# Optimization experiments

Hardware: AMD Instinct MI355X
Metric: run time of the kernel (lower is better)

Reference implementation:

```python
import jax, jax.numpy as jnp
import numpy as np

TOP_K = 2  # matches init_kwargs top_k


def setup_inputs() -> dict:
    key = jax.random.key(0)
    ks = jax.random.split(key, 5)
    B, T, C, H, E = 4, 1024, 768, 3072, 8
    x = jax.random.normal(ks[0], (B, T, C), dtype=jnp.float32)
    Wg = jax.random.normal(ks[1], (C, E), dtype=jnp.float32) * 0.02
    W1 = jax.random.normal(ks[2], (E, C, H), dtype=jnp.float32) * (1.0 / np.sqrt(C))
    b1 = jnp.zeros((E, H), dtype=jnp.float32)
    W2 = jax.random.normal(ks[3], (E, H, C), dtype=jnp.float32) * (1.0 / np.sqrt(H))
    b2 = jnp.zeros((E, C), dtype=jnp.float32)
    return {"x": x, "Wg": Wg, "W1": W1, "b1": b1, "W2": W2, "b2": b2}


def reference(x, Wg, W1, b1, W2, b2):
    # TopKRouter: softmax over expert logits, keep top-k probs, zeros elsewhere.
    E = Wg.shape[-1]
    logits = jnp.einsum('btc,ce->bte', x, Wg)
    probs = jax.nn.softmax(logits, axis=-1)
    top_vals, top_idx = jax.lax.top_k(probs, TOP_K)          # (B,T,K)
    gates = (jax.nn.one_hot(top_idx, E, dtype=probs.dtype) * top_vals[..., None]).sum(-2)  # (B,T,E)

    # Per-expert FFN (Linear -> ReLU -> Linear; dropout is identity in eval),
    # combined with sparse gate weights (only top-k entries are nonzero).
    h = jax.nn.relu(jnp.einsum('btc,ech->bteh', x, W1) + b1)  # (B,T,E,H)
    y = jnp.einsum('bteh,ehc->btec', h, W2) + b2              # (B,T,E,C)
    out = jnp.einsum('bte,btec->btc', gates, y)               # (B,T,C)
    return out
```

## Files before the change

### kernel.cpp

```cpp
#include <hip/hip_runtime.h>
#include <hip/hip_bf16.h>
#include <cmath>

#define NT    4096
#define CDIM  768
#define HDIM  3072
#define NEXP  8
#define CAP   1280

typedef __bf16 bf16_t;
typedef __bf16 bf16x8 __attribute__((ext_vector_type(8)));
typedef float  f32x4  __attribute__((ext_vector_type(4)));

__device__ __forceinline__ void glds16(const void* g, void* l) {
    __builtin_amdgcn_global_load_lds(
        (const __attribute__((address_space(1))) void*)g,
        (__attribute__((address_space(3))) void*)l, 16, 0, 0);
}

template<int R, int CC>
__global__ __launch_bounds__(256)
void transpose_convert_kernel(const float* __restrict__ in, bf16_t* __restrict__ out) {
    __shared__ float tile[64][68];
    int e = blockIdx.z;
    int c0 = blockIdx.x * 64, r0 = blockIdx.y * 64;
    const float* src = in + (size_t)e * R * CC;
    bf16_t* dst = out + (size_t)e * R * CC;
    int t = threadIdx.x;
    int c4 = (t & 15) * 4, rr = t >> 4;
    #pragma unroll
    for (int i = 0; i < 4; i++) {
        int r = rr + i * 16;
        float4 v = *reinterpret_cast<const float4*>(&src[(size_t)(r0 + r) * CC + c0 + c4]);
        tile[r][c4 + 0] = v.x; tile[r][c4 + 1] = v.y;
        tile[r][c4 + 2] = v.z; tile[r][c4 + 3] = v.w;
    }
    __syncthreads();
    #pragma unroll
    for (int i = 0; i < 4; i++) {
        int cc = rr + i * 16;
        int r4 = (t & 15) * 4;
        union { bf16_t h[4]; uint2 u; } un;
        un.h[0] = (bf16_t)tile[r4 + 0][cc]; un.h[1] = (bf16_t)tile[r4 + 1][cc];
        un.h[2] = (bf16_t)tile[r4 + 2][cc]; un.h[3] = (bf16_t)tile[r4 + 3][cc];
        *reinterpret_cast<uint2*>(&dst[(size_t)(c0 + cc) * R + r0 + r4]) = un.u;
    }
}

__global__ __launch_bounds__(512)
void router_kernel(const float* __restrict__ x, const float* __restrict__ wg,
                   bf16_t* __restrict__ xb,
                   int* __restrict__ counts, int* __restrict__ tmap,
                   float* __restrict__ gmap, int* __restrict__ smap) {
    __shared__ int lcnt[NEXP];
    __shared__ int gbase[NEXP];
    int tid = threadIdx.x, lane = tid & 63, wid = tid >> 6;
    if (tid < NEXP) lcnt[tid] = 0;
    __syncthreads();

    int ti0[4], ti1[4], tr0[4], tr1[4];
    float tg0[4], tg1[4];

    #pragma unroll
    for (int k = 0; k < 4; k++) {
        int t = blockIdx.x * 32 + wid * 4 + k;
        const float* xr = x + (size_t)t * CDIM;
        float acc[NEXP];
        #pragma unroll
        for (int e = 0; e < NEXP; e++) acc[e] = 0.f;
        #pragma unroll
        for (int i = 0; i < CDIM / 256; i++) {
            int c = (i * 64 + lane) * 4;
            float4 v = *reinterpret_cast<const float4*>(xr + c);
            union { bf16_t h[4]; uint2 u; } un;
            un.h[0] = (bf16_t)v.x; un.h[1] = (bf16_t)v.y;
            un.h[2] = (bf16_t)v.z; un.h[3] = (bf16_t)v.w;
            *reinterpret_cast<uint2*>(xb + (size_t)t * CDIM + c) = un.u;
            float vv[4] = {v.x, v.y, v.z, v.w};
            #pragma unroll
            for (int j = 0; j < 4; j++)
                #pragma unroll
                for (int e = 0; e < NEXP; e++)
                    acc[e] += vv[j] * wg[(c + j) * NEXP + e];
        }
        #pragma unroll
        for (int e = 0; e < NEXP; e++) {
            #pragma unroll
            for (int off = 32; off > 0; off >>= 1)
                acc[e] += __shfl_xor(acc[e], off, 64);
        }
        if (lane == 0) {
            float mx = acc[0];
            #pragma unroll
            for (int e = 1; e < NEXP; e++) mx = fmaxf(mx, acc[e]);
            float p[NEXP], s = 0.f;
            #pragma unroll
            for (int e = 0; e < NEXP; e++) { p[e] = expf(acc[e] - mx); s += p[e]; }
            float inv = 1.f / s;
            int i0 = 0;
            #pragma unroll
            for (int e = 1; e < NEXP; e++) if (p[e] > p[i0]) i0 = e;
            int i1 = (i0 == 0) ? 1 : 0;
            #pragma unroll
            for (int e = 0; e < NEXP; e++) if (e != i0 && p[e] > p[i1]) i1 = e;
            ti0[k] = i0; ti1[k] = i1;
            tg0[k] = p[i0] * inv; tg1[k] = p[i1] * inv;
            tr0[k] = atomicAdd(&lcnt[i0], 1);
            tr1[k] = atomicAdd(&lcnt[i1], 1);
        }
    }
    __syncthreads();
    if (tid < NEXP) gbase[tid] = atomicAdd(&counts[tid], lcnt[tid]);
    __syncthreads();
    if (lane == 0) {
        #pragma unroll
        for (int k = 0; k < 4; k++) {
            int t = blockIdx.x * 32 + wid * 4 + k;
            int c0 = gbase[ti0[k]] + tr0[k]; if (c0 >= CAP) c0 = CAP - 1;
            int c1 = gbase[ti1[k]] + tr1[k]; if (c1 >= CAP) c1 = CAP - 1;
            int s0 = ti0[k] * CAP + c0, s1 = ti1[k] * CAP + c1;
            tmap[s0] = t; gmap[s0] = tg0[k]; smap[t * 2]     = s0;
            tmap[s1] = t; gmap[s1] = tg1[k]; smap[t * 2 + 1] = s1;
        }
    }
}

__global__ __launch_bounds__(256)
void moe_gemm1_kernel(const bf16_t* __restrict__ xb, const bf16_t* __restrict__ w1t,
                      const float* __restrict__ b1, const int* __restrict__ counts,
                      const int* __restrict__ tmap, bf16_t* __restrict__ hws) {
    int h = blockIdx.x;
    int e = h & 7;
    int local = h >> 3;
    int mt = local / (HDIM / 128);
    int nt = local - mt * (HDIM / 128);
    int cnt = counts[e]; if (cnt > CAP) cnt = CAP;
    if (mt * 128 >= cnt) return;
    int m0 = e * CAP + mt * 128;
    int rend = e * CAP + cnt;
    int n0 = nt * 128;

    __shared__ __attribute__((aligned(16))) bf16_t As[128 * 32];
    __shared__ __attribute__((aligned(16))) bf16_t Bs[128 * 32];

    int tid = threadIdx.x, lane = tid & 63, wid = tid >> 6;
    const bf16_t* aP[2];
    const bf16_t* bP[2];
    int reg[2];
    #pragma unroll
    for (int it = 0; it < 2; it++) {
        int region = wid * 2 + it;
        int row = region * 16 + (lane >> 2);
        int kk = (lane & 3) * 8;
        int pos = m0 + row;
        if (pos > rend - 1) pos = rend - 1;
        aP[it] = xb + (size_t)tmap[pos] * CDIM + kk;
        bP[it] = w1t + ((size_t)e * HDIM + n0 + row) * CDIM + kk;
        reg[it] = region * 512;
    }

    int wm = (wid >> 1) * 64, wn = (wid & 1) * 64;
    int q = lane >> 4, mr = lane & 15;

    f32x4 acc[4][4];
    #pragma unroll
    for (int i = 0; i < 4; i++)
        #pragma unroll
        for (int j = 0; j < 4; j++)
            acc[i][j] = (f32x4){0.f, 0.f, 0.f, 0.f};

    for (int k0 = 0; k0 < CDIM; k0 += 32) {
        #pragma unroll
        for (int it = 0; it < 2; it++) {
            glds16(aP[it] + k0, As + reg[it]);
            glds16(bP[it] + k0, Bs + reg[it]);
        }
        __syncthreads();
        bf16x8 af[4], bfr[4];
        #pragma unroll
        for (int ti = 0; ti < 4; ti++)
            af[ti] = *reinterpret_cast<const bf16x8*>(&As[(wm + ti * 16 + mr) * 32 + q * 8]);
        #pragma unroll
        for (int tj = 0; tj < 4; tj++)
            bfr[tj] = *reinterpret_cast<const bf16x8*>(&Bs[(wn + tj * 16 + mr) * 32 + q * 8]);
        #pragma unroll
        for (int ti = 0; ti < 4; ti++)
            #pragma unroll
            for (int tj = 0; tj < 4; tj++)
                acc[ti][tj] = __builtin_amdgcn_mfma_f32_16x16x32_bf16(af[ti], bfr[tj], acc[ti][tj], 0, 0, 0);
        __syncthreads();
    }

    const float* be = b1 + (size_t)e * HDIM + n0;
    #pragma unroll
    for (int ti = 0; ti < 4; ti++) {
        #pragma unroll
        for (int r = 0; r < 4; r++) {
            int pos = m0 + wm + ti * 16 + q * 4 + r;
            if (pos < rend) {
                bf16_t* hrow = hws + (size_t)pos * HDIM + n0;
                #pragma unroll
                for (int tj = 0; tj < 4; tj++) {
                    float v = acc[ti][tj][r] + be[wn + tj * 16 + mr];
                    hrow[wn + tj * 16 + mr] = (bf16_t)fmaxf(v, 0.f);
                }
            }
        }
    }
}

__global__ __launch_bounds__(256)
void moe_gemm2_kernel(const bf16_t* __restrict__ hws, const bf16_t* __restrict__ w2t,
                      const float* __restrict__ b2, const int* __restrict__ counts,
                      const float* __restrict__ gmap, float* __restrict__ yws) {
    int h = blockIdx.x;
    int e = h & 7;
    int local = h >> 3;
    int mt = local / (CDIM / 128);
    int nt = local - mt * (CDIM / 128);
    int cnt = counts[e]; if (cnt > CAP) cnt = CAP;
    if (mt * 128 >= cnt) return;
    int m0 = e * CAP + mt * 128;
    int rend = e * CAP + cnt;
    int n0 = nt * 128;

    __shared__ __attribute__((aligned(16))) bf16_t As[128 * 32];
    __shared__ __attribute__((aligned(16))) bf16_t Bs[128 * 32];

    int tid = threadIdx.x, lane = tid & 63, wid = tid >> 6;
    const bf16_t* aP[2];
    const bf16_t* bP[2];
    int reg[2];
    #pragma unroll
    for (int it = 0; it < 2; it++) {
        int region = wid * 2 + it;
        int row = region * 16 + (lane >> 2);
        int kk = (lane & 3) * 8;
        int pos = m0 + row;
        if (pos > rend - 1) pos = rend - 1;
        aP[it] = hws + (size_t)pos * HDIM + kk;
        bP[it] = w2t + ((size_t)e * CDIM + n0 + row) * HDIM + kk;
        reg[it] = region * 512;
    }

    int wm = (wid >> 1) * 64, wn = (wid & 1) * 64;
    int q = lane >> 4, mr = lane & 15;

    f32x4 acc[4][4];
    #pragma unroll
    for (int i = 0; i < 4; i++)
        #pragma unroll
        for (int j = 0; j < 4; j++)
            acc[i][j] = (f32x4){0.f, 0.f, 0.f, 0.f};

    for (int k0 = 0; k0 < HDIM; k0 += 32) {
        #pragma unroll
        for (int it = 0; it < 2; it++) {
            glds16(aP[it] + k0, As + reg[it]);
            glds16(bP[it] + k0, Bs + reg[it]);
        }
        __syncthreads();
        bf16x8 af[4], bfr[4];
        #pragma unroll
        for (int ti = 0; ti < 4; ti++)
            af[ti] = *reinterpret_cast<const bf16x8*>(&As[(wm + ti * 16 + mr) * 32 + q * 8]);
        #pragma unroll
        for (int tj = 0; tj < 4; tj++)
            bfr[tj] = *reinterpret_cast<const bf16x8*>(&Bs[(wn + tj * 16 + mr) * 32 + q * 8]);
        #pragma unroll
        for (int ti = 0; ti < 4; ti++)
            #pragma unroll
            for (int tj = 0; tj < 4; tj++)
                acc[ti][tj] = __builtin_amdgcn_mfma_f32_16x16x32_bf16(af[ti], bfr[tj], acc[ti][tj], 0, 0, 0);
        __syncthreads();
    }

    const float* be = b2 + (size_t)e * CDIM + n0;
    #pragma unroll
    for (int ti = 0; ti < 4; ti++) {
        #pragma unroll
        for (int r = 0; r < 4; r++) {
            int pos = m0 + wm + ti * 16 + q * 4 + r;
            if (pos < rend) {
                float g = gmap[pos];
                float* yrow = yws + (size_t)pos * CDIM + n0;
                #pragma unroll
                for (int tj = 0; tj < 4; tj++) {
                    float v = acc[ti][tj][r] + be[wn + tj * 16 + mr];
                    yrow[wn + tj * 16 + mr] = g * v;
                }
            }
        }
    }
}

__global__ __launch_bounds__(256)
void combine_kernel(const float* __restrict__ yws, const int* __restrict__ smap,
                    float* __restrict__ out) {
    int idx = blockIdx.x * 256 + threadIdx.x;
    int t = idx / (CDIM / 4);
    int c = (idx - t * (CDIM / 4)) * 4;
    int s0 = smap[t * 2], s1 = smap[t * 2 + 1];
    float4 a = *reinterpret_cast<const float4*>(yws + (size_t)s0 * CDIM + c);
    float4 b = *reinterpret_cast<const float4*>(yws + (size_t)s1 * CDIM + c);
    float4 o = {a.x + b.x, a.y + b.y, a.z + b.z, a.w + b.w};
    *reinterpret_cast<float4*>(out + (size_t)t * CDIM + c) = o;
}

extern "C" void kernel_launch(void* const* d_in, const int* in_sizes, int n_in,
                              void* d_out, int out_size, void* d_ws, size_t ws_size,
                              hipStream_t stream) {
    const float* x  = (const float*)d_in[0];
    const float* wg = (const float*)d_in[1];
    const float* w1 = (const float*)d_in[2];
    const float* b1 = (const float*)d_in[3];
    const float* w2 = (const float*)d_in[4];
    const float* b2 = (const float*)d_in[5];
    float* out = (float*)d_out;

    char* w = (char*)d_ws;
    size_t off = 0;
    bf16_t* xb  = (bf16_t*)(w + off); off += (size_t)NT * CDIM * 2;
    bf16_t* w1t = (bf16_t*)(w + off); off += (size_t)NEXP * CDIM * HDIM * 2;
    bf16_t* w2t = (bf16_t*)(w + off); off += (size_t)NEXP * CDIM * HDIM * 2;
    bf16_t* hws = (bf16_t*)(w + off); off += (size_t)NEXP * CAP * HDIM * 2;
    float* yws  = (float*)w1t;
    int* counts = (int*)(w + off);  off += 64;
    int* tmap   = (int*)(w + off);  off += (size_t)NEXP * CAP * 4;
    int* smap   = (int*)(w + off);  off += (size_t)NT * 2 * 4;
    float* gmap = (float*)(w + off);

    hipMemsetAsync(counts, 0, NEXP * sizeof(int), stream);

    transpose_convert_kernel<CDIM, HDIM>
        <<<dim3(HDIM / 64, CDIM / 64, NEXP), 256, 0, stream>>>(w1, w1t);
    transpose_convert_kernel<HDIM, CDIM>
        <<<dim3(CDIM / 64, HDIM / 64, NEXP), 256, 0, stream>>>(w2, w2t);
    router_kernel<<<NT / 32, 512, 0, stream>>>(x, wg, xb, counts, tmap, gmap, smap);

    moe_gemm1_kernel<<<8 * (CAP / 128) * (HDIM / 128), 256, 0, stream>>>(
        xb, w1t, b1, counts, tmap, hws);
    moe_gemm2_kernel<<<8 * (CAP / 128) * (CDIM / 128), 256, 0, stream>>>(
        hws, w2t, b2, counts, gmap, yws);
    combine_kernel<<<NT * (CDIM / 4) / 256, 256, 0, stream>>>(yws, smap, out);
}
```

Before: 362.7 us.

## Double K-tile depth to 64 in both MoE GEMMs and stage gemm1 epilogue through LDS

Both expert GEMM kernels now load a 64-wide K slice per iteration instead of 32, halving the number of barrier pairs and loop iterations per output tile. Each lane now loads full 128-byte row segments, which gives more contiguous global reads. Gemm1's epilogue packs bias+ReLU results into bf16 pairs via a lane shuffle, stages them in shared memory, and writes 16-byte vectorized rows to the hidden workspace instead of scattered 2-byte stores. LDS use grows to 32-36 KB per block, which may reduce occupancy, and the 128-byte LDS row stride may cause bank conflicts on fragment reads.

```diff
diff --git a/kernel.cpp b/kernel.cpp
--- a/kernel.cpp
+++ b/kernel.cpp
@@ -140,23 +140,23 @@
     int rend = e * CAP + cnt;
     int n0 = nt * 128;
 
-    __shared__ __attribute__((aligned(16))) bf16_t As[128 * 32];
-    __shared__ __attribute__((aligned(16))) bf16_t Bs[128 * 32];
+    __shared__ __attribute__((aligned(16))) char smem[36864];
+    bf16_t* As = (bf16_t*)smem;
+    bf16_t* Bs = (bf16_t*)(smem + 16384);
 
     int tid = threadIdx.x, lane = tid & 63, wid = tid >> 6;
-    const bf16_t* aP[2];
-    const bf16_t* bP[2];
-    int reg[2];
-    #pragma unroll
-    for (int it = 0; it < 2; it++) {
-        int region = wid * 2 + it;
-        int row = region * 16 + (lane >> 2);
-        int kk = (lane & 3) * 8;
+    const bf16_t* aPj[4];
+    const bf16_t* bPj[4];
+    int regB[4];
+    int kk = (lane & 7) * 8;
+    #pragma unroll
+    for (int j = 0; j < 4; j++) {
+        int row = j * 32 + wid * 8 + (lane >> 3);
         int pos = m0 + row;
         if (pos > rend - 1) pos = rend - 1;
-        aP[it] = xb + (size_t)tmap[pos] * CDIM + kk;
-        bP[it] = w1t + ((size_t)e * HDIM + n0 + row) * CDIM + kk;
-        reg[it] = region * 512;
+        aPj[j] = xb + (size_t)tmap[pos] * CDIM + kk;
+        bPj[j] = w1t + ((size_t)e * HDIM + n0 + row) * CDIM + kk;
+        regB[j] = j * 4096 + wid * 1024;
     }
 
     int wm = (wid >> 1) * 64, wn = (wid & 1) * 64;
@@ -169,42 +169,64 @@
         for (int j = 0; j < 4; j++)
             acc[i][j] = (f32x4){0.f, 0.f, 0.f, 0.f};
 
-    for (int k0 = 0; k0 < CDIM; k0 += 32) {
-        #pragma unroll
-        for (int it = 0; it < 2; it++) {
-            glds16(aP[it] + k0, As + reg[it]);
-            glds16(bP[it] + k0, Bs + reg[it]);
+    for (int k0 = 0; k0 < CDIM; k0 += 64) {
+        #pragma unroll
+        for (int j = 0; j < 4; j++) {
+            glds16(aPj[j] + k0, smem + regB[j]);
+            glds16(bPj[j] + k0, smem + 16384 + regB[j]);
         }
         __syncthreads();
-        bf16x8 af[4], bfr[4];
-        #pragma unroll
-        for (int ti = 0; ti < 4; ti++)
-            af[ti] = *reinterpret_cast<const bf16x8*>(&As[(wm + ti * 16 + mr) * 32 + q * 8]);
-        #pragma unroll
-        for (int tj = 0; tj < 4; tj++)
-            bfr[tj] = *reinterpret_cast<const bf16x8*>(&Bs[(wn + tj * 16 + mr) * 32 + q * 8]);
-        #pragma unroll
-        for (int ti = 0; ti < 4; ti++)
+        #pragma unroll
+        for (int ks = 0; ks < 2; ks++) {
+            bf16x8 af[4], bfr[4];
+            #pragma unroll
+            for (int ti = 0; ti < 4; ti++)
+                af[ti] = *reinterpret_cast<const bf16x8*>(&As[(wm + ti * 16 + mr) * 64 + ks * 32 + q * 8]);
             #pragma unroll
             for (int tj = 0; tj < 4; tj++)
-                acc[ti][tj] = __builtin_amdgcn_mfma_f32_16x16x32_bf16(af[ti], bfr[tj], acc[ti][tj], 0, 0, 0);
+                bfr[tj] = *reinterpret_cast<const bf16x8*>(&Bs[(wn + tj * 16 + mr) * 64 + ks * 32 + q * 8]);
+            #pragma unroll
+            for (int ti = 0; ti < 4; ti++)
+                #pragma unroll
+                for (int tj = 0; tj < 4; tj++)
+                    acc[ti][tj] = __builtin_amdgcn_mfma_f32_16x16x32_bf16(af[ti], bfr[tj], acc[ti][tj], 0, 0, 0);
+        }
         __syncthreads();
     }
 
     const float* be = b1 + (size_t)e * HDIM + n0;
+    float bias[4];
+    #pragma unroll
+    for (int tj = 0; tj < 4; tj++) bias[tj] = be[wn + tj * 16 + mr];
+
+    uint* epw = (uint*)smem + wid * (64 * 36);
     #pragma unroll
     for (int ti = 0; ti < 4; ti++) {
         #pragma unroll
-        for (int r = 0; r < 4; r++) {
-            int pos = m0 + wm + ti * 16 + q * 4 + r;
-            if (pos < rend) {
-                bf16_t* hrow = hws + (size_t)pos * HDIM + n0;
-                #pragma unroll
-                for (int tj = 0; tj < 4; tj++) {
-                    float v = acc[ti][tj][r] + be[wn + tj * 16 + mr];
-                    hrow[wn + tj * 16 + mr] = (bf16_t)fmaxf(v, 0.f);
+        for (int tj = 0; tj < 4; tj++) {
+            #pragma unroll
+            for (int r = 0; r < 4; r++) {
+                float v = fmaxf(acc[ti][tj][r] + bias[tj], 0.f);
+                float o = __shfl_xor(v, 1);
+                if (!(mr & 1)) {
+                    union { bf16_t h[2]; uint u; } pk;
+                    pk.h[0] = (bf16_t)v; pk.h[1] = (bf16_t)o;
+                    int row = ti * 16 + q * 4 + r;
+                    int wd  = tj * 8 + (mr >> 1);
+                    epw[row * 36 + wd] = pk.u;
                 }
             }
+        }
+    }
+    __syncthreads();
+    int c8 = lane & 7;
+    #pragma unroll
+    for (int p = 0; p < 8; p++) {
+        int row = p * 8 + (lane >> 3);
+        int pos = m0 + wm + row;
+        if (pos < rend) {
+            uint4 d = *reinterpret_cast<const uint4*>(&epw[row * 36 + c8 * 4]);
+            *reinterpret_cast<uint4*>(hws + (size_t)pos * HDIM + n0 + wn + c8 * 8) = d;
         }
     }
 }
@@ -224,23 +246,23 @@
     int rend = e * CAP + cnt;
     int n0 = nt * 128;
 
-    __shared__ __attribute__((aligned(16))) bf16_t As[128 * 32];
-    __shared__ __attribute__((aligned(16))) bf16_t Bs[128 * 32];
+    __shared__ __attribute__((aligned(16))) char smem[32768];
+    bf16_t* As = (bf16_t*)smem;
+    bf16_t* Bs = (bf16_t*)(smem + 16384);
 
     int tid = threadIdx.x, lane = tid & 63, wid = tid >> 6;
-    const bf16_t* aP[2];
-    const bf16_t* bP[2];
-    int reg[2];
-    #pragma unroll
-    for (int it = 0; it < 2; it++) {
-        int region = wid * 2 + it;
-        int row = region * 16 + (lane >> 2);
-        int kk = (lane & 3) * 8;
+    const bf16_t* aPj[4];
+    const bf16_t* bPj[4];
+    int regB[4];
+    int kk = (lane & 7) * 8;
+    #pragma unroll
+    for (int j = 0; j < 4; j++) {
+        int row = j * 32 + wid * 8 + (lane >> 3);
         int pos = m0 + row;
         if (pos > rend - 1) pos = rend - 1;
-        aP[it] = hws + (size_t)pos * HDIM + kk;
-        bP[it] = w2t + ((size_t)e * CDIM + n0 + row) * HDIM + kk;
-        reg[it] = region * 512;
+        aPj[j] = hws + (size_t)pos * HDIM + kk;
+        bPj[j] = w2t + ((size_t)e * CDIM + n0 + row) * HDIM + kk;
+        regB[j] = j * 4096 + wid * 1024;
     }
 
     int wm = (wid >> 1) * 64, wn = (wid & 1) * 64;
@@ -253,25 +275,28 @@
         for (int j = 0; j < 4; j++)
             acc[i][j] = (f32x4){0.f, 0.f, 0.f, 0.f};
 
-    for (int k0 = 0; k0 < HDIM; k0 += 32) {
-        #pragma unroll
-        for (int it = 0; it < 2; it++) {
-            glds16(aP[it] + k0, As + reg[it]);
-            glds16(bP[it] + k0, Bs + reg[it]);
+    for (int k0 = 0; k0 < HDIM; k0 += 64) {
+        #pragma unroll
+        for (int j = 0; j < 4; j++) {
+            glds16(aPj[j] + k0, smem + regB[j]);
+            glds16(bPj[j] + k0, smem + 16384 + regB[j]);
         }
         __syncthreads();
-        bf16x8 af[4], bfr[4];
-        #pragma unroll
-        for (int ti = 0; ti < 4; ti++)
-            af[ti] = *reinterpret_cast<const bf16x8*>(&As[(wm + ti * 16 + mr) * 32 + q * 8]);
-        #pragma unroll
-        for (int tj = 0; tj < 4; tj++)
-            bfr[tj] = *reinterpret_cast<const bf16x8*>(&Bs[(wn + tj * 16 + mr) * 32 + q * 8]);
-        #pragma unroll
-        for (int ti = 0; ti < 4; ti++)
+        #pragma unroll
+        for (int ks = 0; ks < 2; ks++) {
+            bf16x8 af[4], bfr[4];
+            #pragma unroll
+            for (int ti = 0; ti < 4; ti++)
+                af[ti] = *reinterpret_cast<const bf16x8*>(&As[(wm + ti * 16 + mr) * 64 + ks * 32 + q * 8]);
             #pragma unroll
             for (int tj = 0; tj < 4; tj++)
-                acc[ti][tj] = __builtin_amdgcn_mfma_f32_16x16x32_bf16(af[ti], bfr[tj], acc[ti][tj], 0, 0, 0);
+                bfr[tj] = *reinterpret_cast<const bf16x8*>(&Bs[(wn + tj * 16 + mr) * 64 + ks * 32 + q * 8]);
+            #pragma unroll
+            for (int ti = 0; ti < 4; ti++)
+                #pragma unroll
+                for (int tj = 0; tj < 4; tj++)
+                    acc[ti][tj] = __builtin_amdgcn_mfma_f32_16x16x32_bf16(af[ti], bfr[tj], acc[ti][tj], 0, 0, 0);
+        }
         __syncthreads();
     }
 
```

Result: slower. 390.9 us (+7.8%).

## Double-buffer LDS tiles in both expert GEMM kernels to overlap loads with MFMA

Applied to the files above, without the earlier changes.

Both expert GEMM kernels now keep two LDS buffers for each of the A and B tiles. The first k-tile is loaded before the loop. Each iteration issues the global-to-LDS loads for the next tile into the other buffer, then runs the MFMAs on the current one. This removes one barrier per iteration and hides global load latency behind compute, at the cost of doubling LDS per block (to 32 KB), which may lower occupancy.

```diff
diff --git a/kernel.cpp b/kernel.cpp
--- a/kernel.cpp
+++ b/kernel.cpp
@@ -140,8 +140,8 @@
     int rend = e * CAP + cnt;
     int n0 = nt * 128;
 
-    __shared__ __attribute__((aligned(16))) bf16_t As[128 * 32];
-    __shared__ __attribute__((aligned(16))) bf16_t Bs[128 * 32];
+    __shared__ __attribute__((aligned(16))) bf16_t As[2][128 * 32];
+    __shared__ __attribute__((aligned(16))) bf16_t Bs[2][128 * 32];
 
     int tid = threadIdx.x, lane = tid & 63, wid = tid >> 6;
     const bf16_t* aP[2];
@@ -169,26 +169,37 @@
         for (int j = 0; j < 4; j++)
             acc[i][j] = (f32x4){0.f, 0.f, 0.f, 0.f};
 
+    #pragma unroll
+    for (int it = 0; it < 2; it++) {
+        glds16(aP[it], &As[0][reg[it]]);
+        glds16(bP[it], &Bs[0][reg[it]]);
+    }
+    __syncthreads();
+
+    int cur = 0;
     for (int k0 = 0; k0 < CDIM; k0 += 32) {
-        #pragma unroll
-        for (int it = 0; it < 2; it++) {
-            glds16(aP[it] + k0, As + reg[it]);
-            glds16(bP[it] + k0, Bs + reg[it]);
-        }
-        __syncthreads();
+        int nk = k0 + 32;
+        if (nk < CDIM) {
+            #pragma unroll
+            for (int it = 0; it < 2; it++) {
+                glds16(aP[it] + nk, &As[cur ^ 1][reg[it]]);
+                glds16(bP[it] + nk, &Bs[cur ^ 1][reg[it]]);
+            }
+        }
         bf16x8 af[4], bfr[4];
         #pragma unroll
         for (int ti = 0; ti < 4; ti++)
-            af[ti] = *reinterpret_cast<const bf16x8*>(&As[(wm + ti * 16 + mr) * 32 + q * 8]);
+            af[ti] = *reinterpret_cast<const bf16x8*>(&As[cur][(wm + ti * 16 + mr) * 32 + q * 8]);
         #pragma unroll
         for (int tj = 0; tj < 4; tj++)
-            bfr[tj] = *reinterpret_cast<const bf16x8*>(&Bs[(wn + tj * 16 + mr) * 32 + q * 8]);
+            bfr[tj] = *reinterpret_cast<const bf16x8*>(&Bs[cur][(wn + tj * 16 + mr) * 32 + q * 8]);
         #pragma unroll
         for (int ti = 0; ti < 4; ti++)
             #pragma unroll
             for (int tj = 0; tj < 4; tj++)
                 acc[ti][tj] = __builtin_amdgcn_mfma_f32_16x16x32_bf16(af[ti], bfr[tj], acc[ti][tj], 0, 0, 0);
         __syncthreads();
+        cur ^= 1;
     }
 
     const float* be = b1 + (size_t)e * HDIM + n0;
@@ -224,8 +235,8 @@
     int rend = e * CAP + cnt;
     int n0 = nt * 128;
 
-    __shared__ __attribute__((aligned(16))) bf16_t As[128 * 32];
-    __shared__ __attribute__((aligned(16))) bf16_t Bs[128 * 32];
+    __shared__ __attribute__((aligned(16))) bf16_t As[2][128 * 32];
+    __shared__ __attribute__((aligned(16))) bf16_t Bs[2][128 * 32];
 
     int tid = threadIdx.x, lane = tid & 63, wid = tid >> 6;
     const bf16_t* aP[2];
@@ -253,26 +264,37 @@
         for (int j = 0; j < 4; j++)
             acc[i][j] = (f32x4){0.f, 0.f, 0.f, 0.f};
 
+    #pragma unroll
+    for (int it = 0; it < 2; it++) {
+        glds16(aP[it], &As[0][reg[it]]);
+        glds16(bP[it], &Bs[0][reg[it]]);
+    }
+    __syncthreads();
+
+    int cur = 0;
     for (int k0 = 0; k0 < HDIM; k0 += 32) {
-        #pragma unroll
-        for (int it = 0; it < 2; it++) {
-            glds16(aP[it] + k0, As + reg[it]);
-            glds16(bP[it] + k0, Bs + reg[it]);
-        }
-        __syncthreads();
+        int nk = k0 + 32;
+        if (nk < HDIM) {
+            #pragma unroll
+            for (int it = 0; it < 2; it++) {
+                glds16(aP[it] + nk, &As[cur ^ 1][reg[it]]);
+                glds16(bP[it] + nk, &Bs[cur ^ 1][reg[it]]);
+            }
+        }
         bf16x8 af[4], bfr[4];
         #pragma unroll
         for (int ti = 0; ti < 4; ti++)
-            af[ti] = *reinterpret_cast<const bf16x8*>(&As[(wm + ti * 16 + mr) * 32 + q * 8]);
+            af[ti] = *reinterpret_cast<const bf16x8*>(&As[cur][(wm + ti * 16 + mr) * 32 + q * 8]);
         #pragma unroll
         for (int tj = 0; tj < 4; tj++)
-            bfr[tj] = *reinterpret_cast<const bf16x8*>(&Bs[(wn + tj * 16 + mr) * 32 + q * 8]);
+            bfr[tj] = *reinterpret_cast<const bf16x8*>(&Bs[cur][(wn + tj * 16 + mr) * 32 + q * 8]);
         #pragma unroll
         for (int ti = 0; ti < 4; ti++)
             #pragma unroll
             for (int tj = 0; tj < 4; tj++)
                 acc[ti][tj] = __builtin_amdgcn_mfma_f32_16x16x32_bf16(af[ti], bfr[tj], acc[ti][tj], 0, 0, 0);
         __syncthreads();
+        cur ^= 1;
     }
 
     const float* be = b2 + (size_t)e * CDIM + n0;
```

Result: no change. 360.4 us (-0.6%).

## Add 4-stage LDS ring with 2-ahead async prefetch in MoE GEMMs

Applied to the files above, without the earlier changes.

Both expert GEMM kernels move from a single LDS buffer, which waited on every global-to-LDS load, to a four-slot ring filled two k-steps ahead using global_load_lds. A manual vmcnt wait plus one barrier per step replaces the two __syncthreads, so memory latency overlaps with MFMA work. LDS use per block grows fourfold to 64KB, which can reduce occupancy. Correctness depends on the hand-counted vmcnt values and on the slot spacing keeping a buffer from being overwritten while other waves still read it.

```diff
diff --git a/kernel.cpp b/kernel.cpp
--- a/kernel.cpp
+++ b/kernel.cpp
@@ -140,8 +140,8 @@
     int rend = e * CAP + cnt;
     int n0 = nt * 128;
 
-    __shared__ __attribute__((aligned(16))) bf16_t As[128 * 32];
-    __shared__ __attribute__((aligned(16))) bf16_t Bs[128 * 32];
+    __shared__ __attribute__((aligned(16))) bf16_t As[4][128 * 32];
+    __shared__ __attribute__((aligned(16))) bf16_t Bs[4][128 * 32];
 
     int tid = threadIdx.x, lane = tid & 63, wid = tid >> 6;
     const bf16_t* aP[2];
@@ -159,6 +159,17 @@
         reg[it] = region * 512;
     }
 
+    #pragma unroll
+    for (int it = 0; it < 2; it++) {
+        glds16(aP[it],      &As[0][reg[it]]);
+        glds16(bP[it],      &Bs[0][reg[it]]);
+    }
+    #pragma unroll
+    for (int it = 0; it < 2; it++) {
+        glds16(aP[it] + 32, &As[1][reg[it]]);
+        glds16(bP[it] + 32, &Bs[1][reg[it]]);
+    }
+
     int wm = (wid >> 1) * 64, wn = (wid & 1) * 64;
     int q = lane >> 4, mr = lane & 15;
 
@@ -169,27 +180,42 @@
         for (int j = 0; j < 4; j++)
             acc[i][j] = (f32x4){0.f, 0.f, 0.f, 0.f};
 
-    for (int k0 = 0; k0 < CDIM; k0 += 32) {
-        #pragma unroll
-        for (int it = 0; it < 2; it++) {
-            glds16(aP[it] + k0, As + reg[it]);
-            glds16(bP[it] + k0, Bs + reg[it]);
-        }
-        __syncthreads();
+    const int NSTEP = CDIM / 32;
+    int rb = 0;
+    for (int t = 0; t < NSTEP; t++) {
+        int sb = rb + 2; if (sb >= 4) sb -= 4;
+        if (t + 2 < NSTEP) {
+            int ko = (t + 2) * 32;
+            #pragma unroll
+            for (int it = 0; it < 2; it++) {
+                glds16(aP[it] + ko, &As[sb][reg[it]]);
+                glds16(bP[it] + ko, &Bs[sb][reg[it]]);
+            }
+            asm volatile("s_waitcnt vmcnt(8)" ::: "memory");
+        } else if (t + 2 == NSTEP) {
+            asm volatile("s_waitcnt vmcnt(4)" ::: "memory");
+        } else {
+            asm volatile("s_waitcnt vmcnt(0)" ::: "memory");
+        }
+        __builtin_amdgcn_s_barrier();
+        __builtin_amdgcn_sched_barrier(0);
+        const bf16_t* Ab = &As[rb][0];
+        const bf16_t* Bb = &Bs[rb][0];
         bf16x8 af[4], bfr[4];
         #pragma unroll
         for (int ti = 0; ti < 4; ti++)
-            af[ti] = *reinterpret_cast<const bf16x8*>(&As[(wm + ti * 16 + mr) * 32 + q * 8]);
+            af[ti] = *reinterpret_cast<const bf16x8*>(&Ab[(wm + ti * 16 + mr) * 32 + q * 8]);
         #pragma unroll
         for (int tj = 0; tj < 4; tj++)
-            bfr[tj] = *reinterpret_cast<const bf16x8*>(&Bs[(wn + tj * 16 + mr) * 32 + q * 8]);
+            bfr[tj] = *reinterpret_cast<const bf16x8*>(&Bb[(wn + tj * 16 + mr) * 32 + q * 8]);
         #pragma unroll
         for (int ti = 0; ti < 4; ti++)
             #pragma unroll
             for (int tj = 0; tj < 4; tj++)
                 acc[ti][tj] = __builtin_amdgcn_mfma_f32_16x16x32_bf16(af[ti], bfr[tj], acc[ti][tj], 0, 0, 0);
-        __syncthreads();
-    }
+        rb = rb + 1; if (rb >= 4) rb -= 4;
+    }
+    __builtin_amdgcn_sched_barrier(0);
 
     const float* be = b1 + (size_t)e * HDIM + n0;
     #pragma unroll
@@ -224,8 +250,8 @@
     int rend = e * CAP + cnt;
     int n0 = nt * 128;
 
-    __shared__ __attribute__((aligned(16))) bf16_t As[128 * 32];
-    __shared__ __attribute__((aligned(16))) bf16_t Bs[128 * 32];
+    __shared__ __attribute__((aligned(16))) bf16_t As[4][128 * 32];
+    __shared__ __attribute__((aligned(16))) bf16_t Bs[4][128 * 32];
 
     int tid = threadIdx.x, lane = tid & 63, wid = tid >> 6;
     const bf16_t* aP[2];
@@ -243,6 +269,17 @@
         reg[it] = region * 512;
     }
 
+    #pragma unroll
+    for (int it = 0; it < 2; it++) {
+        glds16(aP[it],      &As[0][reg[it]]);
+        glds16(bP[it],      &Bs[0][reg[it]]);
+    }
+    #pragma unroll
+    for (int it = 0; it < 2; it++) {
+        glds16(aP[it] + 32, &As[1][reg[it]]);
+        glds16(bP[it] + 32, &Bs[1][reg[it]]);
+    }
+
     int wm = (wid >> 1) * 64, wn = (wid & 1) * 64;
     int q = lane >> 4, mr = lane & 15;
 
@@ -253,27 +290,42 @@
         for (int j = 0; j < 4; j++)
             acc[i][j] = (f32x4){0.f, 0.f, 0.f, 0.f};
 
-    for (int k0 = 0; k0 < HDIM; k0 += 32) {
-        #pragma unroll
-        for (int it = 0; it < 2; it++) {
-            glds16(aP[it] + k0, As + reg[it]);
-            glds16(bP[it] + k0, Bs + reg[it]);
-        }
-        __syncthreads();
+    const int NSTEP = HDIM / 32;
+    int rb = 0;
+    for (int t = 0; t < NSTEP; t++) {
+        int sb = rb + 2; if (sb >= 4) sb -= 4;
+        if (t + 2 < NSTEP) {
+            int ko = (t + 2) * 32;
+            #pragma unroll
+            for (int it = 0; it < 2; it++) {
+                glds16(aP[it] + ko, &As[sb][reg[it]]);
+                glds16(bP[it] + ko, &Bs[sb][reg[it]]);
+            }
+            asm volatile("s_waitcnt vmcnt(8)" ::: "memory");
+        } else if (t + 2 == NSTEP) {
+            asm volatile("s_waitcnt vmcnt(4)" ::: "memory");
+        } else {
+            asm volatile("s_waitcnt vmcnt(0)" ::: "memory");
+        }
+        __builtin_amdgcn_s_barrier();
+        __builtin_amdgcn_sched_barrier(0);
+        const bf16_t* Ab = &As[rb][0];
+        const bf16_t* Bb = &Bs[rb][0];
         bf16x8 af[4], bfr[4];
         #pragma unroll
         for (int ti = 0; ti < 4; ti++)
-            af[ti] = *reinterpret_cast<const bf16x8*>(&As[(wm + ti * 16 + mr) * 32 + q * 8]);
+            af[ti] = *reinterpret_cast<const bf16x8*>(&Ab[(wm + ti * 16 + mr) * 32 + q * 8]);
         #pragma unroll
         for (int tj = 0; tj < 4; tj++)
-            bfr[tj] = *reinterpret_cast<const bf16x8*>(&Bs[(wn + tj * 16 + mr) * 32 + q * 8]);
+            bfr[tj] = *reinterpret_cast<const bf16x8*>(&Bb[(wn + tj * 16 + mr) * 32 + q * 8]);
         #pragma unroll
         for (int ti = 0; ti < 4; ti++)
             #pragma unroll
             for (int tj = 0; tj < 4; tj++)
                 acc[ti][tj] = __builtin_amdgcn_mfma_f32_16x16x32_bf16(af[ti], bfr[tj], acc[ti][tj], 0, 0, 0);
-        __syncthreads();
-    }
+        rb = rb + 1; if (rb >= 4) rb -= 4;
+    }
+    __builtin_amdgcn_sched_barrier(0);
 
     const float* be = b2 + (size_t)e * CDIM + n0;
     #pragma unroll
```

Result: no change. 366.1 us (+1.0%).
